# Performance work log

Measured on AMD Instinct MI355X. Metric: run time of the kernel, lower is better.

## Reference

```python
import jax, jax.numpy as jnp
import numpy as np

B, C, H, W = 8, 8, 512, 512

# one-pixel shifts with zero padding (equivalent to the bmm with shift matrices)
def shift_right(x):  # out[..., c] = x[..., c-1]
    return jnp.pad(x, ((0, 0), (0, 0), (1, 0)))[:, :, :-1]
def shift_left(x):   # out[..., c] = x[..., c+1]
    return jnp.pad(x, ((0, 0), (0, 0), (0, 1)))[:, :, 1:]
def shift_up(x):     # out[r] = x[r+1]
    return jnp.pad(x, ((0, 0), (0, 1), (0, 0)))[:, 1:, :]
def shift_down(x):   # out[r] = x[r-1]
    return jnp.pad(x, ((0, 0), (1, 0), (0, 0)))[:, :-1, :]

def bilater_voting(c):
    # c: [B, 8, H, W] probabilities
    right        = shift_right(c[:, 4])
    left         = shift_left(c[:, 3])
    left_bottom  = shift_left(shift_down(c[:, 5]))
    right_above  = shift_right(shift_up(c[:, 2]))
    left_above   = shift_left(shift_up(c[:, 0]))
    bottom       = shift_down(c[:, 6])
    up           = shift_up(c[:, 1])
    right_bottom = shift_right(shift_down(c[:, 7]))
    a1 = c[:, 3] * right
    a2 = c[:, 4] * left
    a3 = c[:, 1] * bottom
    a4 = c[:, 6] * up
    a5 = c[:, 2] * left_bottom
    a6 = c[:, 5] * right_above
    a7 = c[:, 0] * right_bottom
    a8 = c[:, 7] * left_above
    vote_out = jnp.stack([a7, a3, a5, a1, a2, a6, a4, a8], axis=1)
    glo_map = jnp.mean(vote_out, axis=1)
    return glo_map, vote_out

def bce(p, t):
    # matches torch F.binary_cross_entropy (mean reduction, log clamped at -100)
    logp = jnp.clip(jnp.log(p), -100.0, None)
    log1mp = jnp.clip(jnp.log(1.0 - p), -100.0, None)
    return -jnp.mean(t * logp + (1.0 - t) * log1mp)

def setup_inputs() -> dict:
    key = jax.random.key(0)
    k1, k2, k3, k4 = jax.random.split(key, 4)
    atts = jax.random.normal(k1, (B, C, H, W), dtype=jnp.float32)
    dets = jax.random.normal(k2, (B, C, H, W), dtype=jnp.float32)
    target = jax.random.randint(k3, (B, 1, H, W), 0, 2).astype(jnp.float32)
    con_target = jax.random.randint(k4, (B, C, H, W), 0, 2).astype(jnp.float32)
    return {"atts": atts, "dets": dets, "target": target, "con_target": con_target}

def reference(atts, dets, target, con_target):
    # edge mask from connectivity GT: pixels with 0 < sum < 8
    sum_conn = jnp.sum(con_target, axis=1)  # [B, H, W]
    edge_conn = jnp.where((sum_conn < 8.0) & (sum_conn > 0.0), 1.0, 0.0)

    atts_p = jax.nn.sigmoid(atts)
    dets_p = jax.nn.sigmoid(dets)

    glo_map1, vote_out1 = bilater_voting(atts_p)
    glo_map2, vote_out2 = bilater_voting(dets_p)

    # edge/decouple loss on dets branch
    pred_mask_min = 1.0 - jnp.min(vote_out2, axis=1)
    pred_mask_min = pred_mask_min * edge_conn
    decouple_map = glo_map2 * (1.0 - edge_conn) + pred_mask_min
    de_loss2 = bce(decouple_map[:, None], target)

    bce_loss1 = bce(glo_map1[:, None], target)
    bicon_loss1 = bce(vote_out1, con_target)
    conn_loss1 = bce(atts_p, con_target)
    bicon_loss2 = bce(vote_out2, con_target)
    conn_loss2 = bce(dets_p, con_target)

    loss = (0.2 * bicon_loss1 + 0.8 * conn_loss1 + bce_loss1
            + 0.2 * bicon_loss2 + 0.8 * conn_loss2 + de_loss2)
    return loss
```

## Files before the change

kernel.cpp:

```cpp
#include <hip/hip_runtime.h>
#include <stdint.h>

#define BB 8
#define CC 8
#define HH 512
#define WW 512
#define HWSZ (HH * WW)

typedef float v4 __attribute__((ext_vector_type(4)));

#define LOG2_CLAMP -144.26950409f

__device__ __forceinline__ v4 uload4(const float* __restrict__ p) {
    v4 r;
    __builtin_memcpy(&r, p, sizeof(v4));
    return r;
}
__device__ __forceinline__ v4 aload4(const float* __restrict__ p) {
    return *(const v4* __restrict__)p;
}

__device__ __forceinline__ v4 sig4(v4 x) {
    v4 r;
#pragma unroll
    for (int i = 0; i < 4; ++i)
        r[i] = __builtin_amdgcn_rcpf(1.0f + __expf(-x[i]));
    return r;
}

__device__ __forceinline__ void gload_lds16(const float* g, float* l) {
    __builtin_amdgcn_global_load_lds(
        (const __attribute__((address_space(1))) void*)g,
        (__attribute__((address_space(3))) void*)l, 16, 0, 0);
}

__global__ __launch_bounds__(256, 4) void bicon_loss_kernel(
    const float* __restrict__ atts, const float* __restrict__ dets,
    const float* __restrict__ target, const float* __restrict__ con,
    float* __restrict__ out)
{
    __shared__ __align__(16) float an_lds[8][4][256];

    const int nchunk = (int)gridDim.x >> 3;
    const int bid = ((int)blockIdx.x & 7) * nchunk + ((int)blockIdx.x >> 3);

    const int tid  = (int)threadIdx.x;
    const int idx  = bid * 256 + tid;
    const int w0   = (idx & 127) << 2;
    const int row  = idx >> 7;
    const int h    = row & (HH - 1);
    const int b    = row >> 9;
    const int lane = tid & 63;
    const int wid  = tid >> 6;

    const int hm = (h > 0) ? h - 1 : 0;
    const int hp = (h < HH - 1) ? h + 1 : HH - 1;
    const float mh0 = (h > 0) ? 1.0f : 0.0f;
    const float mh1 = (h < HH - 1) ? 1.0f : 0.0f;
    const float mw0 = (w0 == 0) ? 0.0f : 1.0f;
    const float mw3 = (w0 == WW - 4) ? 0.0f : 1.0f;

    const int offC = h * WW + w0;
    const int offU = hm * WW + w0;
    const int offD = hp * WW + w0;

    const float* __restrict__ ab = atts + b * CC * HWSZ;
    const float* __restrict__ db = dets + b * CC * HWSZ;
    const float* __restrict__ cb = con  + b * CC * HWSZ;

    gload_lds16(ab + 7 * HWSZ + offU - 1, &an_lds[0][wid][0]);
    gload_lds16(ab + 6 * HWSZ + offU    , &an_lds[1][wid][0]);
    gload_lds16(ab + 5 * HWSZ + offU + 1, &an_lds[2][wid][0]);
    gload_lds16(ab + 4 * HWSZ + offC - 1, &an_lds[3][wid][0]);
    gload_lds16(ab + 3 * HWSZ + offC + 1, &an_lds[4][wid][0]);
    gload_lds16(ab + 2 * HWSZ + offD - 1, &an_lds[5][wid][0]);
    gload_lds16(ab + 1 * HWSZ + offD    , &an_lds[6][wid][0]);
    gload_lds16(ab + 0 * HWSZ + offD + 1, &an_lds[7][wid][0]);

    v4 dc[8], dn[8], ac[8];
#pragma unroll
    for (int c = 0; c < 8; ++c) dc[c] = aload4(db + c * HWSZ + offC);
    dn[0] = uload4(db + 7 * HWSZ + offU - 1);
    dn[1] = aload4(db + 6 * HWSZ + offU);
    dn[2] = uload4(db + 5 * HWSZ + offU + 1);
    dn[3] = uload4(db + 4 * HWSZ + offC - 1);
    dn[4] = uload4(db + 3 * HWSZ + offC + 1);
    dn[5] = uload4(db + 2 * HWSZ + offD - 1);
    dn[6] = aload4(db + 1 * HWSZ + offD);
    dn[7] = uload4(db + 0 * HWSZ + offD + 1);
#pragma unroll
    for (int c = 0; c < 8; ++c) ac[c] = aload4(ab + c * HWSZ + offC);

    uint32_t sel = 0u;
#pragma unroll
    for (int c = 0; c < 8; ++c) {
        v4 cvv = aload4(cb + c * HWSZ + offC);
#pragma unroll
        for (int i = 0; i < 4; ++i)
            if (cvv[i] > 0.5f) sel |= (1u << (c * 4 + i));
    }
    v4 tv = aload4(target + b * HWSZ + offC);
    uint32_t tb = 0u;
#pragma unroll
    for (int i = 0; i < 4; ++i)
        if (tv[i] > 0.5f) tb |= (1u << i);

    const float mkA[8] = {mh0 * mw0, mh0, mh0,       mw0, 1.f, mh1 * mw0, mh1, mh1};
    const float mkB[8] = {mh0,       mh0, mh0,       1.f, 1.f, mh1,       mh1, mh1};
    const float mkC[8] = {mh0,       mh0, mh0 * mw3, 1.f, mw3, mh1,       mh1, mh1 * mw3};

    const v4 one = {1.f, 1.f, 1.f, 1.f};

    v4 pb0 = one, pb1 = one, pc = one;
    v4 vsum = {0.f, 0.f, 0.f, 0.f};
    v4 vmin = {1e30f, 1e30f, 1e30f, 1e30f};
#pragma unroll
    for (int k = 0; k < 8; ++k) {
        v4 s = sig4(dc[k]);
        v4 n = sig4(dn[k]);
        n[0] *= mkA[k]; n[1] *= mkB[k]; n[2] *= mkB[k]; n[3] *= mkC[k];
        v4 v = s * n;
        vsum += v;
        vmin = __builtin_elementwise_min(vmin, v);
        v4 av, as;
#pragma unroll
        for (int i = 0; i < 4; ++i) {
            const bool bt = (sel >> (k * 4 + i)) & 1u;
            av[i] = bt ? v[i] : 1.0f - v[i];
            as[i] = bt ? s[i] : 1.0f - s[i];
        }
        if (k < 4) pb0 *= av; else pb1 *= av;
        pc *= as;
    }
    const v4 glo2  = vsum * 0.125f;
    const v4 vmin2 = vmin;
    float Lb2 = 0.f, Lc2 = 0.f;
#pragma unroll
    for (int i = 0; i < 4; ++i) {
        Lb2 += fmaxf(__log2f(pb0[i]), LOG2_CLAMP) + fmaxf(__log2f(pb1[i]), LOG2_CLAMP);
        Lc2 += fmaxf(__log2f(pc[i]), LOG2_CLAMP);
    }

    asm volatile("s_waitcnt vmcnt(0)" ::: "memory");

    v4 qb0 = one, qb1 = one, qc = one;
    v4 qsum = {0.f, 0.f, 0.f, 0.f};
#pragma unroll
    for (int k = 0; k < 8; ++k) {
        v4 s = sig4(ac[k]);
        v4 n = sig4(*(const v4*)&an_lds[k][wid][lane * 4]);
        n[0] *= mkA[k]; n[1] *= mkB[k]; n[2] *= mkB[k]; n[3] *= mkC[k];
        v4 v = s * n;
        qsum += v;
        v4 av, as;
#pragma unroll
        for (int i = 0; i < 4; ++i) {
            const bool bt = (sel >> (k * 4 + i)) & 1u;
            av[i] = bt ? v[i] : 1.0f - v[i];
            as[i] = bt ? s[i] : 1.0f - s[i];
        }
        if (k < 4) qb0 *= av; else qb1 *= av;
        qc *= as;
    }
    const v4 glo1 = qsum * 0.125f;
    float Lb1 = 0.f, Lc1 = 0.f;
#pragma unroll
    for (int i = 0; i < 4; ++i) {
        Lb1 += fmaxf(__log2f(qb0[i]), LOG2_CLAMP) + fmaxf(__log2f(qb1[i]), LOG2_CLAMP);
        Lc1 += fmaxf(__log2f(qc[i]), LOG2_CLAMP);
    }

    float Lp = 0.f;
#pragma unroll
    for (int i = 0; i < 4; ++i) {
        const uint32_t mI    = 0x11111111u << i;
        const uint32_t bitsI = sel & mI;
        const bool edge = (bitsI != 0u) && (bitsI != mI);
        const float dec = edge ? (1.0f - vmin2[i]) : glo2[i];
        const bool  ti  = (tb >> i) & 1u;
        const float a   = ti ? glo1[i] : 1.0f - glo1[i];
        const float bs  = ti ? dec     : 1.0f - dec;
        Lp += fmaxf(__log2f(a * bs), LOG2_CLAMP);
    }

    const float wbic = 0.2f / (float)(BB * CC * HWSZ);
    const float wcon = 0.8f / (float)(BB * CC * HWSZ);
    const float wpix = 1.0f / (float)(BB * HWSZ);
    const float ln2  = 0.69314718056f;

    float local = -(wbic * (Lb1 + Lb2) + wcon * (Lc1 + Lc2) + wpix * Lp) * ln2;

#pragma unroll
    for (int off = 32; off > 0; off >>= 1)
        local += __shfl_down(local, off, 64);

    __shared__ float wsum[4];
    if (lane == 0) wsum[wid] = local;
    __syncthreads();
    if (tid == 0) {
        atomicAdd(out, wsum[0] + wsum[1] + wsum[2] + wsum[3]);
    }
}

extern "C" void kernel_launch(void* const* d_in, const int* in_sizes, int n_in,
                              void* d_out, int out_size, void* d_ws, size_t ws_size,
                              hipStream_t stream) {
    const float* atts   = (const float*)d_in[0];
    const float* dets   = (const float*)d_in[1];
    const float* target = (const float*)d_in[2];
    const float* con    = (const float*)d_in[3];
    float* out = (float*)d_out;

    hipMemsetAsync(out, 0, sizeof(float), stream);

    const int ngroups = BB * HH * WW / 4;
    bicon_loss_kernel<<<ngroups / 256, 256, 0, stream>>>(atts, dets, target, con, out);
}
```

Measured before the change: 208.8 us.

## Stage 2D halo tiles in LDS for both branches instead of redundant shifted loads

Each block now processes a 16x64 pixel tile. It stages all 8 channels of atts (then dets) with a one-row, one-column halo into shared memory, and shifted neighbour values are read from there. This replaces the per-thread unaligned global loads of shifted dets rows and the per-row LDS staging of atts. The aim is to cut redundant global traffic, at the cost of larger LDS use, lower occupancy (launch bound 3), extra block barriers and serialized staging of the two inputs.

```diff
diff --git a/kernel.cpp b/kernel.cpp
--- a/kernel.cpp
+++ b/kernel.cpp
@@ -11,13 +11,11 @@
 
 #define LOG2_CLAMP -144.26950409f
 
-__device__ __forceinline__ v4 uload4(const float* __restrict__ p) {
-    v4 r;
-    __builtin_memcpy(&r, p, sizeof(v4));
-    return r;
-}
 __device__ __forceinline__ v4 aload4(const float* __restrict__ p) {
     return *(const v4* __restrict__)p;
+}
+__device__ __forceinline__ v4 lds4(const float* p) {
+    return *(const v4*)p;
 }
 
 __device__ __forceinline__ v4 sig4(v4 x) {
@@ -34,94 +32,72 @@
         (__attribute__((address_space(3))) void*)l, 16, 0, 0);
 }
 
-__global__ __launch_bounds__(256, 4) void bicon_loss_kernel(
-    const float* __restrict__ atts, const float* __restrict__ dets,
-    const float* __restrict__ target, const float* __restrict__ con,
-    float* __restrict__ out)
+__device__ __forceinline__ void stage_tile(
+    const float* __restrict__ ib, float* sC, v4* sH,
+    int tid, int row0, int col0)
 {
-    __shared__ __align__(16) float an_lds[8][4][256];
-
-    const int nchunk = (int)gridDim.x >> 3;
-    const int bid = ((int)blockIdx.x & 7) * nchunk + ((int)blockIdx.x >> 3);
-
-    const int tid  = (int)threadIdx.x;
-    const int idx  = bid * 256 + tid;
-    const int w0   = (idx & 127) << 2;
-    const int row  = idx >> 7;
-    const int h    = row & (HH - 1);
-    const int b    = row >> 9;
-    const int lane = tid & 63;
-    const int wid  = tid >> 6;
-
-    const int hm = (h > 0) ? h - 1 : 0;
-    const int hp = (h < HH - 1) ? h + 1 : HH - 1;
-    const float mh0 = (h > 0) ? 1.0f : 0.0f;
-    const float mh1 = (h < HH - 1) ? 1.0f : 0.0f;
-    const float mw0 = (w0 == 0) ? 0.0f : 1.0f;
-    const float mw3 = (w0 == WW - 4) ? 0.0f : 1.0f;
-
-    const int offC = h * WW + w0;
-    const int offU = hm * WW + w0;
-    const int offD = hp * WW + w0;
-
-    const float* __restrict__ ab = atts + b * CC * HWSZ;
-    const float* __restrict__ db = dets + b * CC * HWSZ;
-    const float* __restrict__ cb = con  + b * CC * HWSZ;
-
-    gload_lds16(ab + 7 * HWSZ + offU - 1, &an_lds[0][wid][0]);
-    gload_lds16(ab + 6 * HWSZ + offU    , &an_lds[1][wid][0]);
-    gload_lds16(ab + 5 * HWSZ + offU + 1, &an_lds[2][wid][0]);
-    gload_lds16(ab + 4 * HWSZ + offC - 1, &an_lds[3][wid][0]);
-    gload_lds16(ab + 3 * HWSZ + offC + 1, &an_lds[4][wid][0]);
-    gload_lds16(ab + 2 * HWSZ + offD - 1, &an_lds[5][wid][0]);
-    gload_lds16(ab + 1 * HWSZ + offD    , &an_lds[6][wid][0]);
-    gload_lds16(ab + 0 * HWSZ + offD + 1, &an_lds[7][wid][0]);
-
-    v4 dc[8], dn[8], ac[8];
-#pragma unroll
-    for (int c = 0; c < 8; ++c) dc[c] = aload4(db + c * HWSZ + offC);
-    dn[0] = uload4(db + 7 * HWSZ + offU - 1);
-    dn[1] = aload4(db + 6 * HWSZ + offU);
-    dn[2] = uload4(db + 5 * HWSZ + offU + 1);
-    dn[3] = uload4(db + 4 * HWSZ + offC - 1);
-    dn[4] = uload4(db + 3 * HWSZ + offC + 1);
-    dn[5] = uload4(db + 2 * HWSZ + offD - 1);
-    dn[6] = aload4(db + 1 * HWSZ + offD);
-    dn[7] = uload4(db + 0 * HWSZ + offD + 1);
-#pragma unroll
-    for (int c = 0; c < 8; ++c) ac[c] = aload4(ab + c * HWSZ + offC);
-
-    uint32_t sel = 0u;
-#pragma unroll
-    for (int c = 0; c < 8; ++c) {
-        v4 cvv = aload4(cb + c * HWSZ + offC);
-#pragma unroll
-        for (int i = 0; i < 4; ++i)
-            if (cvv[i] > 0.5f) sel |= (1u << (c * 4 + i));
-    }
-    v4 tv = aload4(target + b * HWSZ + offC);
-    uint32_t tb = 0u;
-#pragma unroll
-    for (int i = 0; i < 4; ++i)
-        if (tv[i] > 0.5f) tb |= (1u << i);
-
-    const float mkA[8] = {mh0 * mw0, mh0, mh0,       mw0, 1.f, mh1 * mw0, mh1, mh1};
-    const float mkB[8] = {mh0,       mh0, mh0,       1.f, 1.f, mh1,       mh1, mh1};
-    const float mkC[8] = {mh0,       mh0, mh0 * mw3, 1.f, mw3, mh1,       mh1, mh1 * mw3};
-
+#pragma unroll
+    for (int i = 0; i < 9; ++i) {
+        const unsigned j  = (unsigned)(i * 256 + tid);
+        const unsigned ch = j / 288u;
+        const unsigned r  = (j - ch * 288u) >> 4;
+        const unsigned cv = j & 15u;
+        int gr = row0 - 1 + (int)r;
+        gr = min(max(gr, 0), HH - 1);
+        gload_lds16(ib + ch * HWSZ + gr * WW + col0 + cv * 4, sC + j * 4);
+    }
+    const int colL = max(col0 - 4, 0);
+    const int colR = min(col0 + 64, WW - 4);
+#pragma unroll
+    for (int l = 0; l < 2; ++l) {
+        const unsigned j    = (unsigned)(l * 256 + tid);
+        const unsigned ch   = j >> 6;
+        const unsigned side = (j >> 5) & 1u;
+        const unsigned r    = j & 31u;
+        int gr = row0 - 1 + (int)min(r, 17u);
+        gr = min(max(gr, 0), HH - 1);
+        if (r < 18u)
+            gload_lds16(ib + ch * HWSZ + gr * WW + (side ? colR : colL),
+                        (float*)(sH + j));
+    }
+}
+
+template <bool NEED_MIN>
+__device__ __forceinline__ void eval_prod(
+    const float* sC, const v4* sH, int tx, int ty, uint32_t sel,
+    const float* mkA, const float* mkB, const float* mkC,
+    v4& pb0o, v4& pb1o, v4& pco, v4& glo, v4& vminO)
+{
     const v4 one = {1.f, 1.f, 1.f, 1.f};
-
     v4 pb0 = one, pb1 = one, pc = one;
     v4 vsum = {0.f, 0.f, 0.f, 0.f};
     v4 vmin = {1e30f, 1e30f, 1e30f, 1e30f};
+    const int NCH[8] = {7, 6, 5, 4, 3, 2, 1, 0};
+    const int DR[8]  = {0, 0, 0, 1, 1, 2, 2, 2};
+    const int SS[8]  = {-1, 0, 1, -1, 1, -1, 0, 1};
 #pragma unroll
     for (int k = 0; k < 8; ++k) {
-        v4 s = sig4(dc[k]);
-        v4 n = sig4(dn[k]);
+        v4 s = sig4(lds4(sC + k * 1152 + (ty + 1) * 64 + tx * 4));
+        const int ch = NCH[k];
+        const float* rowp = sC + ch * 1152 + (ty + DR[k]) * 64;
+        v4 qc = lds4(rowp + tx * 4);
+        v4 nraw;
+        if (SS[k] == 0) {
+            nraw = qc;
+        } else if (SS[k] < 0) {
+            v4 qp = (tx > 0) ? lds4(rowp + tx * 4 - 4)
+                             : sH[(ch * 2 + 0) * 32 + (ty + DR[k])];
+            nraw = __builtin_shufflevector(qp, qc, 3, 4, 5, 6);
+        } else {
+            v4 qn = (tx < 15) ? lds4(rowp + tx * 4 + 4)
+                              : sH[(ch * 2 + 1) * 32 + (ty + DR[k])];
+            nraw = __builtin_shufflevector(qc, qn, 1, 2, 3, 4);
+        }
+        v4 n = sig4(nraw);
         n[0] *= mkA[k]; n[1] *= mkB[k]; n[2] *= mkB[k]; n[3] *= mkC[k];
         v4 v = s * n;
         vsum += v;
-        vmin = __builtin_elementwise_min(vmin, v);
+        if (NEED_MIN) vmin = __builtin_elementwise_min(vmin, v);
         v4 av, as;
 #pragma unroll
         for (int i = 0; i < 4; ++i) {
@@ -132,42 +108,96 @@
         if (k < 4) pb0 *= av; else pb1 *= av;
         pc *= as;
     }
-    const v4 glo2  = vsum * 0.125f;
-    const v4 vmin2 = vmin;
+    pb0o = pb0; pb1o = pb1; pco = pc;
+    glo = vsum * 0.125f;
+    if (NEED_MIN) vminO = vmin;
+}
+
+__global__ __launch_bounds__(256, 3) void bicon_loss_kernel(
+    const float* __restrict__ atts, const float* __restrict__ dets,
+    const float* __restrict__ target, const float* __restrict__ con,
+    float* __restrict__ out)
+{
+    __shared__ __align__(16) float sC[8 * 18 * 64];
+    __shared__ __align__(16) v4    sH[512];
+    __shared__ float wsum[4];
+
+    const int nchunk = (int)gridDim.x >> 3;
+    const int bid = ((int)blockIdx.x & 7) * nchunk + ((int)blockIdx.x >> 3);
+
+    const int tid  = (int)threadIdx.x;
+    const int colt = bid & 7;
+    const int band = (bid >> 3) & 31;
+    const int b    = bid >> 8;
+    const int row0 = band << 4;
+    const int col0 = colt << 6;
+    const int tx = tid & 15;
+    const int ty = tid >> 4;
+    const int h  = row0 + ty;
+    const int w0 = col0 + (tx << 2);
+    const int lane = tid & 63;
+    const int wid  = tid >> 6;
+
+    const float mh0 = (h > 0) ? 1.0f : 0.0f;
+    const float mh1 = (h < HH - 1) ? 1.0f : 0.0f;
+    const float mw0 = (w0 == 0) ? 0.0f : 1.0f;
+    const float mw3 = (w0 == WW - 4) ? 0.0f : 1.0f;
+
+    const float* __restrict__ ab = atts + b * CC * HWSZ;
+    const float* __restrict__ db = dets + b * CC * HWSZ;
+    const float* __restrict__ cb = con  + b * CC * HWSZ;
+    const int offC = h * WW + w0;
+
+    v4 cvv[8];
+#pragma unroll
+    for (int c = 0; c < 8; ++c) cvv[c] = aload4(cb + c * HWSZ + offC);
+    v4 tv = aload4(target + b * HWSZ + offC);
+
+    stage_tile(ab, sC, sH, tid, row0, col0);
+
+    uint32_t sel = 0u;
+#pragma unroll
+    for (int c = 0; c < 8; ++c)
+#pragma unroll
+        for (int i = 0; i < 4; ++i)
+            if (cvv[c][i] > 0.5f) sel |= (1u << (c * 4 + i));
+    uint32_t tb = 0u;
+#pragma unroll
+    for (int i = 0; i < 4; ++i)
+        if (tv[i] > 0.5f) tb |= (1u << i);
+
+    const float mkA[8] = {mh0 * mw0, mh0, mh0,       mw0, 1.f, mh1 * mw0, mh1, mh1};
+    const float mkB[8] = {mh0,       mh0, mh0,       1.f, 1.f, mh1,       mh1, mh1};
+    const float mkC[8] = {mh0,       mh0, mh0 * mw3, 1.f, mw3, mh1,       mh1, mh1 * mw3};
+
+    asm volatile("s_waitcnt vmcnt(0)" ::: "memory");
+    __syncthreads();
+
+    v4 pb0_1, pb1_1, pc_1, glo1, vdum;
+    eval_prod<false>(sC, sH, tx, ty, sel, mkA, mkB, mkC,
+                     pb0_1, pb1_1, pc_1, glo1, vdum);
+
+    __syncthreads();
+    stage_tile(db, sC, sH, tid, row0, col0);
+
+    float Lb1 = 0.f, Lc1 = 0.f;
+#pragma unroll
+    for (int i = 0; i < 4; ++i) {
+        Lb1 += fmaxf(__log2f(pb0_1[i]), LOG2_CLAMP) + fmaxf(__log2f(pb1_1[i]), LOG2_CLAMP);
+        Lc1 += fmaxf(__log2f(pc_1[i]), LOG2_CLAMP);
+    }
+
+    asm volatile("s_waitcnt vmcnt(0)" ::: "memory");
+    __syncthreads();
+
+    v4 pb0_2, pb1_2, pc_2, glo2, vmin2;
+    eval_prod<true>(sC, sH, tx, ty, sel, mkA, mkB, mkC,
+                    pb0_2, pb1_2, pc_2, glo2, vmin2);
     float Lb2 = 0.f, Lc2 = 0.f;
 #pragma unroll
     for (int i = 0; i < 4; ++i) {
-        Lb2 += fmaxf(__log2f(pb0[i]), LOG2_CLAMP) + fmaxf(__log2f(pb1[i]), LOG2_CLAMP);
-        Lc2 += fmaxf(__log2f(pc[i]), LOG2_CLAMP);
-    }
-
-    asm volatile("s_waitcnt vmcnt(0)" ::: "memory");
-
-    v4 qb0 = one, qb1 = one, qc = one;
-    v4 qsum = {0.f, 0.f, 0.f, 0.f};
-#pragma unroll
-    for (int k = 0; k < 8; ++k) {
-        v4 s = sig4(ac[k]);
-        v4 n = sig4(*(const v4*)&an_lds[k][wid][lane * 4]);
-        n[0] *= mkA[k]; n[1] *= mkB[k]; n[2] *= mkB[k]; n[3] *= mkC[k];
-        v4 v = s * n;
-        qsum += v;
-        v4 av, as;
-#pragma unroll
-        for (int i = 0; i < 4; ++i) {
-            const bool bt = (sel >> (k * 4 + i)) & 1u;
-            av[i] = bt ? v[i] : 1.0f - v[i];
-            as[i] = bt ? s[i] : 1.0f - s[i];
-        }
-        if (k < 4) qb0 *= av; else qb1 *= av;
-        qc *= as;
-    }
-    const v4 glo1 = qsum * 0.125f;
-    float Lb1 = 0.f, Lc1 = 0.f;
-#pragma unroll
-    for (int i = 0; i < 4; ++i) {
-        Lb1 += fmaxf(__log2f(qb0[i]), LOG2_CLAMP) + fmaxf(__log2f(qb1[i]), LOG2_CLAMP);
-        Lc1 += fmaxf(__log2f(qc[i]), LOG2_CLAMP);
+        Lb2 += fmaxf(__log2f(pb0_2[i]), LOG2_CLAMP) + fmaxf(__log2f(pb1_2[i]), LOG2_CLAMP);
+        Lc2 += fmaxf(__log2f(pc_2[i]), LOG2_CLAMP);
     }
 
     float Lp = 0.f;
@@ -194,7 +224,6 @@
     for (int off = 32; off > 0; off >>= 1)
         local += __shfl_down(local, off, 64);
 
-    __shared__ float wsum[4];
     if (lane == 0) wsum[wid] = local;
     __syncthreads();
     if (tid == 0) {
@@ -213,6 +242,6 @@
 
     hipMemsetAsync(out, 0, sizeof(float), stream);
 
-    const int ngroups = BB * HH * WW / 4;
-    bicon_loss_kernel<<<ngroups / 256, 256, 0, stream>>>(atts, dets, target, con, out);
-}
+    const int nblocks = BB * (HH / 16) * (WW / 64);
+    bicon_loss_kernel<<<nblocks, 256, 0, stream>>>(atts, dets, target, con, out);
+}
```

Result: no change. 207.7 us (-0.5%).
